# Kernel tuning notes

Hardware: AMD Instinct MI355X
Metric: run time of the kernel (lower is better)

## Reference

```python
import jax, jax.numpy as jnp
import numpy as np

B, E, R, A, NV, SEL = 512, 1024, 1024, 512, 196, 36

def _lstm_cell(x, h, c, Wih, bih, Whh, bhh):
    g = x @ Wih.T + bih + h @ Whh.T + bhh
    i, f, gg, o = jnp.split(g, 4, axis=1)  # torch gate order i,f,g,o
    c2 = jax.nn.sigmoid(f) * c + jax.nn.sigmoid(i) * jnp.tanh(gg)
    h2 = jax.nn.sigmoid(o) * jnp.tanh(c2)
    return h2, c2

def _attention(h, feats, p_feats, Wh, bh, Wa, ba):
    # feats: [B,S,R], p_feats: [B,S,A]
    att_h = h @ Wh.T + bh                       # [B,A]
    dot = jnp.tanh(p_feats + att_h[:, None, :])  # [B,S,A]
    scores = jnp.einsum('bsa,a->bs', dot, Wa[0]) + ba[0]
    w = jax.nn.softmax(scores, axis=1)
    return jnp.einsum('bs,bsd->bd', w, feats)

def setup_inputs() -> dict:
    key = jax.random.key(0)
    ks = jax.random.split(key, 32)
    s = 0.02
    inp = {
        'xt': jax.random.normal(ks[0], (B, E), jnp.float32),
        'fc_feats': jax.random.normal(ks[1], (B, R), jnp.float32),
        'att_feats': jax.random.normal(ks[2], (B, NV, R), jnp.float32),
        'p_att_feats': jax.random.normal(ks[3], (B, NV, A), jnp.float32),
        'state_h': jax.random.normal(ks[4], (2, B, R), jnp.float32),
        'state_c': jax.random.normal(ks[5], (2, B, R), jnp.float32),
        # att_lstm: input E + 2R
        'W_ih_att': jax.random.normal(ks[6], (4 * R, E + 2 * R), jnp.float32) * s,
        'b_ih_att': jnp.zeros((4 * R,), jnp.float32),
        'W_hh_att': jax.random.normal(ks[7], (4 * R, R), jnp.float32) * s,
        'b_hh_att': jnp.zeros((4 * R,), jnp.float32),
        # lang_lstm: input 3R
        'W_ih_lang': jax.random.normal(ks[8], (4 * R, 3 * R), jnp.float32) * s,
        'b_ih_lang': jnp.zeros((4 * R,), jnp.float32),
        'W_hh_lang': jax.random.normal(ks[9], (4 * R, R), jnp.float32) * s,
        'b_hh_lang': jnp.zeros((4 * R,), jnp.float32),
        # attention 1
        'Wh2att1': jax.random.normal(ks[10], (A, R), jnp.float32) * s,
        'bh2att1': jnp.zeros((A,), jnp.float32),
        'Walpha1': jax.random.normal(ks[11], (1, A), jnp.float32) * s,
        'balpha1': jnp.zeros((1,), jnp.float32),
        # vf attention
        'Wh2att2': jax.random.normal(ks[12], (A, R), jnp.float32) * s,
        'bh2att2': jnp.zeros((A,), jnp.float32),
        'Walpha2': jax.random.normal(ks[13], (1, A), jnp.float32) * s,
        'balpha2': jnp.zeros((1,), jnp.float32),
        # vf_layer and p_vf
        'W_vf': jax.random.normal(ks[14], (NV, 2 * R), jnp.float32) * s,
        'b_vf': jnp.zeros((NV,), jnp.float32),
        'W_pvf': jax.random.normal(ks[15], (A, R), jnp.float32) * s,
        'b_pvf': jnp.zeros((A,), jnp.float32),
    }
    return inp

def reference(xt, fc_feats, att_feats, p_att_feats, state_h, state_c,
              W_ih_att, b_ih_att, W_hh_att, b_hh_att,
              W_ih_lang, b_ih_lang, W_hh_lang, b_hh_lang,
              Wh2att1, bh2att1, Walpha1, balpha1,
              Wh2att2, bh2att2, Walpha2, balpha2,
              W_vf, b_vf, W_pvf, b_pvf):
    # dropout in eval mode -> identity
    prev_h = state_h[-1]
    att_lstm_input = jnp.concatenate([prev_h, fc_feats, xt], axis=1)
    h_att, c_att = _lstm_cell(att_lstm_input, state_h[0], state_c[0],
                              W_ih_att, b_ih_att, W_hh_att, b_hh_att)
    att = _attention(h_att, att_feats, p_att_feats, Wh2att1, bh2att1, Walpha1, balpha1)
    conc = jnp.concatenate([att, h_att], axis=1)          # [B,2R]
    vf_ha = conc @ W_vf.T + b_vf                          # [B,NV]
    vf_soft = jax.nn.softmax(vf_ha, axis=1)
    _, vf_ix = jax.lax.top_k(vf_soft, SEL)                # [B,SEL] (descending)
    arr1 = jnp.take_along_axis(att_feats, vf_ix[:, :, None], axis=1)  # [B,SEL,R]
    p_vf_feats = arr1 @ W_pvf.T + b_pvf                   # [B,SEL,A]
    vf_att = _attention(h_att, arr1, p_vf_feats, Wh2att2, bh2att2, Walpha2, balpha2)
    lang_lstm_input = jnp.concatenate([vf_att, h_att, att], axis=1)
    h_lang, c_lang = _lstm_cell(lang_lstm_input, state_h[1], state_c[1],
                                W_ih_lang, b_ih_lang, W_hh_lang, b_hh_lang)
    output = h_lang
    new_h = jnp.stack([h_att, h_lang])
    new_c = jnp.stack([c_att, c_lang])
    return output, new_h, new_c
```

## Files before the change

### kernel.cpp

```cpp
#include <hip/hip_runtime.h>

typedef __attribute__((ext_vector_type(4))) float f32x4;
typedef __attribute__((ext_vector_type(8))) _Float16 half8;
typedef __attribute__((ext_vector_type(4))) _Float16 half4;

__device__ __forceinline__ float fast_tanh(float x) {
  float e = __expf(2.f * x);
  return 1.f - 2.f / (e + 1.f);
}
__device__ __forceinline__ float fast_sigmoid(float x) {
  return 1.f / (1.f + __expf(-x));
}

__device__ __forceinline__ void gl_lds16(const _Float16* g, _Float16* l) {
  __builtin_amdgcn_global_load_lds(
      (const __attribute__((address_space(1))) void*)g,
      (__attribute__((address_space(3))) void*)l, 16, 0, 0);
}

template<int SPLIT, int OUT16, int NGUARD>
__global__ __launch_bounds__(256) void gemm16(
    const _Float16* __restrict__ Ahp, const _Float16* __restrict__ Alp, int lda,
    const _Float16* __restrict__ Bhp, const _Float16* __restrict__ Blp, int ldb,
    void* __restrict__ Cp, int ldc, long czstride,
    int N, int Kc)
{
  __shared__ _Float16 sAh[128 * 32];
  __shared__ _Float16 sBh[128 * 32];
  __shared__ _Float16 sAl[SPLIT == 3 ? 128 * 32 : 8];
  __shared__ _Float16 sBl[SPLIT == 3 ? 128 * 32 : 8];

  const int tid = threadIdx.x, lane = tid & 63, wid = tid >> 6;
  const int wm = wid >> 1, wn = wid & 1;
  const int l16 = lane & 15, k8 = lane >> 4;
  const int srow = lane >> 2;
  const int scol = (lane & 3) * 8;

  const int  kt0   = blockIdx.z * Kc;
  const long abase = (long)blockIdx.y * 128;
  const long bbase = (long)blockIdx.x * 128;

  const int r0 = wid * 32 + srow;
  const int r1 = wid * 32 + 16 + srow;
  long br0 = bbase + r0, br1 = bbase + r1;
  if (NGUARD) {
    if (br0 > N - 1) br0 = N - 1;
    if (br1 > N - 1) br1 = N - 1;
  }

  const _Float16* ga0 = Ahp + (abase + r0) * (long)lda + kt0 + scol;
  const _Float16* ga1 = Ahp + (abase + r1) * (long)lda + kt0 + scol;
  const _Float16* gb0 = Bhp + br0 * (long)ldb + kt0 + scol;
  const _Float16* gb1 = Bhp + br1 * (long)ldb + kt0 + scol;
  const _Float16* la0 = SPLIT == 3 ? Alp + (abase + r0) * (long)lda + kt0 + scol : nullptr;
  const _Float16* la1 = SPLIT == 3 ? Alp + (abase + r1) * (long)lda + kt0 + scol : nullptr;
  const _Float16* lb0 = SPLIT == 3 ? Blp + br0 * (long)ldb + kt0 + scol : nullptr;
  const _Float16* lb1 = SPLIT == 3 ? Blp + br1 * (long)ldb + kt0 + scol : nullptr;

  const int e0 = (wid * 32) * 32;
  const int e1 = (wid * 32 + 16) * 32;

  f32x4 acc[4][4];
#pragma unroll
  for (int i = 0; i < 4; i++)
#pragma unroll
    for (int j = 0; j < 4; j++) acc[i][j] = (f32x4){0.f, 0.f, 0.f, 0.f};

  for (int kk = 0; kk < Kc; kk += 32) {
    gl_lds16(ga0 + kk, sAh + e0);
    gl_lds16(ga1 + kk, sAh + e1);
    gl_lds16(gb0 + kk, sBh + e0);
    gl_lds16(gb1 + kk, sBh + e1);
    if (SPLIT == 3) {
      gl_lds16(la0 + kk, sAl + e0);
      gl_lds16(la1 + kk, sAl + e1);
      gl_lds16(lb0 + kk, sBl + e0);
      gl_lds16(lb1 + kk, sBl + e1);
    }
    __syncthreads();

    half8 ah[4], bh[4];
#pragma unroll
    for (int m = 0; m < 4; m++)
      ah[m] = *(const half8*)&sAh[(wm * 64 + m * 16 + l16) * 32 + k8 * 8];
#pragma unroll
    for (int n = 0; n < 4; n++)
      bh[n] = *(const half8*)&sBh[(wn * 64 + n * 16 + l16) * 32 + k8 * 8];
#pragma unroll
    for (int m = 0; m < 4; m++)
#pragma unroll
      for (int n = 0; n < 4; n++)
        acc[m][n] = __builtin_amdgcn_mfma_f32_16x16x32_f16(ah[m], bh[n], acc[m][n], 0, 0, 0);
    if (SPLIT == 3) {
      half8 al[4], bl[4];
#pragma unroll
      for (int m = 0; m < 4; m++)
        al[m] = *(const half8*)&sAl[(wm * 64 + m * 16 + l16) * 32 + k8 * 8];
#pragma unroll
      for (int n = 0; n < 4; n++)
        bl[n] = *(const half8*)&sBl[(wn * 64 + n * 16 + l16) * 32 + k8 * 8];
#pragma unroll
      for (int m = 0; m < 4; m++)
#pragma unroll
        for (int n = 0; n < 4; n++) {
          acc[m][n] = __builtin_amdgcn_mfma_f32_16x16x32_f16(al[m], bh[n], acc[m][n], 0, 0, 0);
          acc[m][n] = __builtin_amdgcn_mfma_f32_16x16x32_f16(ah[m], bl[n], acc[m][n], 0, 0, 0);
        }
    }
    __syncthreads();
  }

  const long czoff = (long)blockIdx.z * czstride;
#pragma unroll
  for (int m = 0; m < 4; m++)
#pragma unroll
    for (int n = 0; n < 4; n++) {
      const long row0 = abase + wm * 64 + m * 16 + (lane >> 4) * 4;
      const long col  = bbase + wn * 64 + n * 16 + l16;
      if (!NGUARD || col < N) {
#pragma unroll
        for (int j = 0; j < 4; j++) {
          if (OUT16) ((_Float16*)Cp)[(row0 + j) * (long)ldc + col + czoff] = (_Float16)acc[m][n][j];
          else       ((float*)Cp)[(row0 + j) * (long)ldc + col + czoff] = acc[m][n][j];
        }
      }
    }
}

__global__ __launch_bounds__(256) void pack_kernel(
    const float* __restrict__ xt, const float* __restrict__ fc,
    const float* __restrict__ sh,
    _Float16* __restrict__ X1h, _Float16* __restrict__ X1l)
{
  int i = blockIdx.x * 256 + threadIdx.x;
  int b = i >> 10, rr = i & 1023;
  long base = (long)b * 4096;
  float v[4];
  v[0] = sh[524288 + i];
  v[1] = fc[i];
  v[2] = xt[i];
  v[3] = sh[i];
#pragma unroll
  for (int j = 0; j < 4; j++) {
    _Float16 h = (_Float16)v[j];
    X1h[base + j * 1024 + rr] = h;
    X1l[base + j * 1024 + rr] = (_Float16)(v[j] - (float)h);
  }
}

__global__ __launch_bounds__(256) void convertA_kernel(
    const float* __restrict__ WihA, const float* __restrict__ WhhA,
    const float* __restrict__ Wh1, const float* __restrict__ Wh2,
    const float* __restrict__ Wvf, const float* __restrict__ Wpvf,
    _Float16* __restrict__ WcAh, _Float16* __restrict__ WcAl,
    _Float16* __restrict__ W12h, _Float16* __restrict__ Wvfh,
    _Float16* __restrict__ Wvfl, _Float16* __restrict__ Wpvfh)
{
  int bi = blockIdx.x, t = threadIdx.x;
  if (bi < 16384) {
    long e = ((long)bi * 256 + t) * 4;
    int row = (int)(e >> 12), col = (int)(e & 4095);
    const float* src = (col < 3072) ? WihA + (long)row * 3072 + col
                                    : WhhA + (long)row * 1024 + (col - 3072);
    f32x4 v = *(const f32x4*)src;
    half4 h, l;
#pragma unroll
    for (int j = 0; j < 4; j++) { h[j] = (_Float16)v[j]; l[j] = (_Float16)(v[j] - (float)h[j]); }
    *(half4*)&WcAh[e] = h;
    *(half4*)&WcAl[e] = l;
  } else if (bi < 17408) {
    long e = ((long)(bi - 16384) * 256 + t) * 4;
    int row = (int)(e >> 10), col = (int)(e & 1023);
    const float* src = (row < 512) ? Wh1 + (long)row * 1024 + col
                                   : Wh2 + (long)(row - 512) * 1024 + col;
    f32x4 v = *(const f32x4*)src;
    half4 h;
#pragma unroll
    for (int j = 0; j < 4; j++) h[j] = (_Float16)v[j];
    *(half4*)&W12h[e] = h;
  } else if (bi < 17800) {
    long e = ((long)(bi - 17408) * 256 + t) * 4;
    f32x4 v = *(const f32x4*)(Wvf + e);
    half4 h, l;
#pragma unroll
    for (int j = 0; j < 4; j++) { h[j] = (_Float16)v[j]; l[j] = (_Float16)(v[j] - (float)h[j]); }
    *(half4*)&Wvfh[e] = h;
    *(half4*)&Wvfl[e] = l;
  } else {
    long e = ((long)(bi - 17800) * 256 + t) * 4;
    f32x4 v = *(const f32x4*)(Wpvf + e);
    half4 h;
#pragma unroll
    for (int j = 0; j < 4; j++) h[j] = (_Float16)v[j];
    *(half4*)&Wpvfh[e] = h;
  }
}

__global__ __launch_bounds__(256) void convertL_kernel(
    const float* __restrict__ WihL, const float* __restrict__ WhhL,
    _Float16* __restrict__ WcLh)
{
  long e = ((long)blockIdx.x * 256 + threadIdx.x) * 4;
  int row = (int)(e >> 12), col = (int)(e & 4095);
  const float* src = (col < 3072) ? WihL + (long)row * 3072 + col
                                  : WhhL + (long)row * 1024 + (col - 3072);
  f32x4 v = *(const f32x4*)src;
  half4 h;
#pragma unroll
  for (int j = 0; j < 4; j++) h[j] = (_Float16)v[j];
  *(half4*)&WcLh[e] = h;
}

template<int NP, bool H16, bool ATT>
__global__ __launch_bounds__(256) void lstm_act_kernel(
    const void* __restrict__ gp, const float* __restrict__ bih,
    const float* __restrict__ bhh, const float* __restrict__ cin,
    float* __restrict__ hOut, float* __restrict__ cOut,
    _Float16* __restrict__ hatt_h, _Float16* __restrict__ conch,
    _Float16* __restrict__ concl, float* __restrict__ hOut2)
{
  const long S = 2097152;
  int i = blockIdx.x * 256 + threadIdx.x;
  int b = i >> 10, rr = i & 1023;
  long gb = (long)b * 4096;
  float g4[4];
#pragma unroll
  for (int q = 0; q < 4; q++) {
    float s = 0.f;
#pragma unroll
    for (int z = 0; z < NP; z++) {
      long off = (long)z * S + gb + q * 1024 + rr;
      s += H16 ? (float)((const _Float16*)gp)[off] : ((const float*)gp)[off];
    }
    g4[q] = s + bih[q * 1024 + rr] + bhh[q * 1024 + rr];
  }
  float c  = cin[i];
  float c2 = fast_sigmoid(g4[1]) * c + fast_sigmoid(g4[0]) * fast_tanh(g4[2]);
  float h2 = fast_sigmoid(g4[3]) * fast_tanh(c2);
  hOut[i] = h2;
  cOut[i] = c2;
  if (hOut2) hOut2[i] = h2;
  if (ATT) {
    _Float16 hh = (_Float16)h2;
    hatt_h[i] = hh;
    conch[(long)b * 2048 + 1024 + rr] = hh;
    concl[(long)b * 2048 + 1024 + rr] = (_Float16)(h2 - (float)hh);
  }
}

__global__ __launch_bounds__(256) void x2fill_kernel(
    const float* __restrict__ hatt, const float* __restrict__ sh,
    _Float16* __restrict__ x2h)
{
  int i = blockIdx.x * 256 + threadIdx.x;
  int b = i >> 10, rr = i & 1023;
  x2h[(long)b * 4096 + 1024 + rr] = (_Float16)hatt[i];
  x2h[(long)b * 4096 + 3072 + rr] = (_Float16)sh[524288 + i];
}

__global__ __launch_bounds__(256) void reduce_atth_kernel(
    const float* __restrict__ p, float* __restrict__ o)
{
  int i = (blockIdx.x * 256 + threadIdx.x) * 4;
  f32x4 a = *(const f32x4*)(p + i);
  f32x4 b = *(const f32x4*)(p + 524288 + i);
  f32x4 c = *(const f32x4*)(p + 1048576 + i);
  f32x4 d = *(const f32x4*)(p + 1572864 + i);
  *(f32x4*)(o + i) = a + b + c + d;
}

template<bool EXTRA, bool PF16>
__global__ __launch_bounds__(256) void score_kernel(
    const void* __restrict__ pf, const float* __restrict__ atth,
    const float* __restrict__ bh, const float* __restrict__ extra,
    const float* __restrict__ walpha, const float* __restrict__ balpha,
    float* __restrict__ out, int S, int nrows)
{
  int gw = blockIdx.x * 4 + (threadIdx.x >> 6);
  int lane = threadIdx.x & 63;
  if (gw >= nrows) return;
  int b = gw / S;
  const float* ah = atth + (long)b * 1024 + lane * 8;
  const float* bp = bh + lane * 8;
  const float* wp = walpha + lane * 8;
  const float* ep = EXTRA ? extra + lane * 8 : nullptr;
  float pv[8];
  if (PF16) {
    half8 hv = *(const half8*)((const _Float16*)pf + (long)gw * 512 + lane * 8);
#pragma unroll
    for (int j = 0; j < 8; j++) pv[j] = (float)hv[j];
  } else {
    const float* p = (const float*)pf + (long)gw * 512 + lane * 8;
#pragma unroll
    for (int u = 0; u < 2; u++) { f32x4 t = *(const f32x4*)(p + u * 4);
#pragma unroll
      for (int j = 0; j < 4; j++) pv[u * 4 + j] = t[j]; }
  }
  float acc = 0.f;
#pragma unroll
  for (int u = 0; u < 2; u++) {
    f32x4 av = *(const f32x4*)(ah + u * 4);
    f32x4 bv = *(const f32x4*)(bp + u * 4);
    f32x4 wv = *(const f32x4*)(wp + u * 4);
    f32x4 ev = EXTRA ? *(const f32x4*)(ep + u * 4) : (f32x4){0.f, 0.f, 0.f, 0.f};
#pragma unroll
    for (int j = 0; j < 4; j++) {
      float x = pv[u * 4 + j] + av[j] + bv[j] + ev[j];
      acc += fast_tanh(x) * wv[j];
    }
  }
#pragma unroll
  for (int off = 32; off; off >>= 1) acc += __shfl_xor(acc, off);
  if (lane == 0) out[gw] = acc + balpha[0];
}

__global__ __launch_bounds__(256) void attsum1_kernel(
    const float* __restrict__ scores, const float* __restrict__ feats,
    _Float16* __restrict__ conch, _Float16* __restrict__ concl, _Float16* __restrict__ x2h)
{
  __shared__ float w[256];
  int b = blockIdx.x, t = threadIdx.x;
  float s0 = (t < 196) ? scores[b * 196 + t] : -3.0e38f;
  w[t] = s0;
  __syncthreads();
  float mx = -3.0e38f;
  for (int i = 0; i < 196; i++) mx = fmaxf(mx, w[i]);
  float sum = 0.f;
  for (int i = 0; i < 196; i++) sum += __expf(w[i] - mx);
  float inv = 1.f / sum;
  __syncthreads();
  if (t < 196) w[t] = __expf(s0 - mx) * inv;
  __syncthreads();
  f32x4 acc = (f32x4){0.f, 0.f, 0.f, 0.f};
  const float* fb = feats + (long)b * 200704 + t * 4;
  for (int s0i = 0; s0i < 192; s0i += 8) {
    f32x4 v[8];
#pragma unroll
    for (int u = 0; u < 8; u++) v[u] = *(const f32x4*)(fb + (long)(s0i + u) * 1024);
#pragma unroll
    for (int u = 0; u < 8; u++) {
      float ws = w[s0i + u];
#pragma unroll
      for (int j = 0; j < 4; j++) acc[j] += ws * v[u][j];
    }
  }
#pragma unroll
  for (int u = 192; u < 196; u++) {
    float ws = w[u];
    f32x4 v = *(const f32x4*)(fb + (long)u * 1024);
#pragma unroll
    for (int j = 0; j < 4; j++) acc[j] += ws * v[j];
  }
  half4 h, l;
#pragma unroll
  for (int j = 0; j < 4; j++) { h[j] = (_Float16)acc[j]; l[j] = (_Float16)(acc[j] - (float)h[j]); }
  *(half4*)&conch[(long)b * 2048 + t * 4] = h;
  *(half4*)&concl[(long)b * 2048 + t * 4] = l;
  *(half4*)&x2h[(long)b * 4096 + 2048 + t * 4] = h;
}

__global__ __launch_bounds__(256) void attsum2_kernel(
    const float* __restrict__ scores, const _Float16* __restrict__ arr1h,
    _Float16* __restrict__ x2h)
{
  __shared__ float w[64];
  int b = blockIdx.x, t = threadIdx.x;
  if (t < 64) w[t] = (t < 36) ? scores[b * 36 + t] : -3.0e38f;
  __syncthreads();
  float mx = -3.0e38f;
  for (int i = 0; i < 36; i++) mx = fmaxf(mx, w[i]);
  float sum = 0.f;
  for (int i = 0; i < 36; i++) sum += __expf(w[i] - mx);
  float inv = 1.f / sum;
  __syncthreads();
  if (t < 36) w[t] = __expf(w[t] - mx) * inv;
  __syncthreads();
  f32x4 acc = (f32x4){0.f, 0.f, 0.f, 0.f};
  const _Float16* fb = arr1h + (long)b * 36 * 1024 + t * 4;
#pragma unroll 4
  for (int s = 0; s < 36; s++) {
    float ws = w[s];
    half4 v = *(const half4*)(fb + (long)s * 1024);
#pragma unroll
    for (int j = 0; j < 4; j++) acc[j] += ws * (float)v[j];
  }
  half4 h;
#pragma unroll
  for (int j = 0; j < 4; j++) h[j] = (_Float16)acc[j];
  *(half4*)&x2h[(long)b * 4096 + t * 4] = h;
}

__global__ __launch_bounds__(64) void topk_kernel(
    const float* __restrict__ vfp, const float* __restrict__ b_vf, int* __restrict__ ix)
{
  int b = blockIdx.x;
  int lane = threadIdx.x;
  float v[4];
#pragma unroll
  for (int j = 0; j < 4; j++) {
    int s = lane + 64 * j;
    float sum = -3.0e38f;
    if (s < 196) {
      sum = b_vf[s];
#pragma unroll
      for (int z = 0; z < 8; z++) sum += vfp[(long)z * 100352 + b * 196 + s];
    }
    v[j] = sum;
  }
  for (int it = 0; it < 36; it++) {
    float bv = -3.0e38f; int bs = 1 << 20;
#pragma unroll
    for (int j = 0; j < 4; j++) {
      int s = lane + 64 * j;
      if (v[j] > bv) { bv = v[j]; bs = s; }
    }
#pragma unroll
    for (int off = 32; off; off >>= 1) {
      float ov = __shfl_xor(bv, off);
      int   os = __shfl_xor(bs, off);
      if (ov > bv || (ov == bv && os < bs)) { bv = ov; bs = os; }
    }
    if ((bs & 63) == lane) v[bs >> 6] = -3.0e38f;
    if (lane == 0) ix[b * 36 + it] = bs;
  }
}

__global__ __launch_bounds__(256) void gather_conv_kernel(
    const float* __restrict__ feats, const int* __restrict__ ix, _Float16* __restrict__ dst)
{
  int bj = blockIdx.x;
  int b = bj / 36;
  int s = ix[bj];
  int t = threadIdx.x;
  f32x4 v = *(const f32x4*)(feats + ((long)b * 196 + s) * 1024 + t * 4);
  half4 h;
#pragma unroll
  for (int j = 0; j < 4; j++) h[j] = (_Float16)v[j];
  *(half4*)&dst[(long)bj * 1024 + t * 4] = h;
}

extern "C" void kernel_launch(void* const* d_in, const int* in_sizes, int n_in,
                              void* d_out, int out_size, void* d_ws, size_t ws_size,
                              hipStream_t stream) {
  const float* xt        = (const float*)d_in[0];
  const float* fc_feats  = (const float*)d_in[1];
  const float* att_feats = (const float*)d_in[2];
  const float* p_att     = (const float*)d_in[3];
  const float* state_h   = (const float*)d_in[4];
  const float* state_c   = (const float*)d_in[5];
  const float* b_ih_att  = (const float*)d_in[7];
  const float* b_hh_att  = (const float*)d_in[9];
  const float* b_ih_lang = (const float*)d_in[11];
  const float* b_hh_lang = (const float*)d_in[13];
  const float* bh2att1   = (const float*)d_in[15];
  const float* Walpha1   = (const float*)d_in[16];
  const float* balpha1   = (const float*)d_in[17];
  const float* bh2att2   = (const float*)d_in[19];
  const float* Walpha2   = (const float*)d_in[20];
  const float* balpha2   = (const float*)d_in[21];
  const float* b_vf      = (const float*)d_in[23];
  const float* b_pvf     = (const float*)d_in[25];

  float* out = (float*)d_out;
  float* W = (float*)d_ws;

  _Float16* WcAh   = (_Float16*)(W + 0);
  _Float16* WcAl   = (_Float16*)(W + 8388608);
  _Float16* X1h    = (_Float16*)(W + 16777216);
  _Float16* X1l    = (_Float16*)(W + 17825792);
  float*    g1p    = W + 18874368;
  _Float16* hatt_h = (_Float16*)(W + 27262976);
  _Float16* W12h   = (_Float16*)(W + 27525120);
  _Float16* Wvfh   = (_Float16*)(W + 28049408);
  _Float16* Wvfl   = (_Float16*)(W + 28250112);
  _Float16* Wpvfh  = (_Float16*)(W + 28450816);
  _Float16* WcLh   = WcAh;
  float*    vfhap  = W + 8388608;
  _Float16* arr1h  = (_Float16*)(W + 8388608);
  _Float16* g2ph   = (_Float16*)(W + 8388608);
  _Float16* conch  = (_Float16*)(W + 17825792);
  _Float16* concl  = (_Float16*)(W + 18350080);
  int*      vfix   = (int*)(W + 17825792);
  float*    scores2= W + 17844224;
  float*    atthp  = W + 18874368;
  float*    atth   = W + 20971520;
  _Float16* X2h    = (_Float16*)(W + 21495808);
  float*    scores1= W + 22544384;
  _Float16* pvf16  = (_Float16*)(W + 22544384);

  float* out_h0 = out + 524288;
  float* out_h1 = out + 2 * 524288;
  float* out_c0 = out + 3 * 524288;
  float* out_c1 = out + 4 * 524288;

  pack_kernel<<<2048, 256, 0, stream>>>(xt, fc_feats, state_h, X1h, X1l);

  convertA_kernel<<<18312, 256, 0, stream>>>(
      (const float*)d_in[6], (const float*)d_in[8],
      (const float*)d_in[14], (const float*)d_in[18],
      (const float*)d_in[22], (const float*)d_in[24],
      WcAh, WcAl, W12h, Wvfh, Wvfl, Wpvfh);

  gemm16<3, 0, 0><<<dim3(32, 4, 4), 256, 0, stream>>>(
      X1h, X1l, 4096, WcAh, WcAl, 4096, g1p, 4096, 2097152, 4096, 1024);

  lstm_act_kernel<4, false, true><<<2048, 256, 0, stream>>>(
      g1p, b_ih_att, b_hh_att, state_c, out_h0, out_c0,
      hatt_h, conch, concl, nullptr);

  x2fill_kernel<<<2048, 256, 0, stream>>>(out_h0, state_h, X2h);

  convertL_kernel<<<16384, 256, 0, stream>>>(
      (const float*)d_in[10], (const float*)d_in[12], WcLh);

  gemm16<1, 0, 0><<<dim3(8, 4, 4), 256, 0, stream>>>(
      hatt_h, nullptr, 1024, W12h, nullptr, 1024, atthp, 1024, 524288, 1024, 256);
  reduce_atth_kernel<<<512, 256, 0, stream>>>(atthp, atth);

  score_kernel<false, false><<<25088, 256, 0, stream>>>(
      p_att, atth, bh2att1, nullptr, Walpha1, balpha1, scores1, 196, 100352);

  attsum1_kernel<<<512, 256, 0, stream>>>(scores1, att_feats, conch, concl, X2h);

  gemm16<3, 0, 1><<<dim3(2, 4, 8), 256, 0, stream>>>(
      conch, concl, 2048, Wvfh, Wvfl, 2048, vfhap, 196, 100352, 196, 256);

  topk_kernel<<<512, 64, 0, stream>>>(vfhap, b_vf, vfix);

  gather_conv_kernel<<<18432, 256, 0, stream>>>(att_feats, vfix, arr1h);

  gemm16<1, 1, 0><<<dim3(4, 144, 1), 256, 0, stream>>>(
      arr1h, nullptr, 1024, Wpvfh, nullptr, 1024, pvf16, 512, 0, 512, 1024);

  score_kernel<true, true><<<4608, 256, 0, stream>>>(
      pvf16, atth + 512, bh2att2, b_pvf, Walpha2, balpha2, scores2, 36, 18432);

  attsum2_kernel<<<512, 256, 0, stream>>>(scores2, arr1h, X2h);

  gemm16<1, 1, 0><<<dim3(32, 4, 8), 256, 0, stream>>>(
      X2h, nullptr, 4096, WcLh, nullptr, 4096, g2ph, 4096, 2097152, 4096, 512);

  lstm_act_kernel<8, true, false><<<2048, 256, 0, stream>>>(
      g2ph, b_ih_lang, b_hh_lang, state_c + 524288, out, out_c1,
      nullptr, nullptr, nullptr, out_h1);
}
```

Before: 443.8 us.

## Add double-buffered full-M GEMM for LSTM gates, swizzle LDS, fuse vf attention

Adds a gemm_big kernel for the two big LSTM gate GEMMs. It uses 512 threads, a tile covering all 512 rows by 64 columns, double-buffered LDS staging and a 4-way K split, so each weight tile is read once and loads overlap the MFMA work. LDS column addressing is XOR-swizzled in both GEMMs to cut bank conflicts. The vf score and softmax-sum kernels are fused into one, and the vf GEMM split-K is raised from 8 to 16 with topk summing more partials. Other changes are a swapped grid order for the pvf GEMM and moving convertL earlier. Risks are lower occupancy from the large LDS footprint and more partial-sum traffic.

```diff
diff --git a/kernel.cpp b/kernel.cpp
--- a/kernel.cpp
+++ b/kernel.cpp
@@ -18,7 +18,107 @@
       (__attribute__((address_space(3))) void*)l, 16, 0, 0);
 }
 
-template<int SPLIT, int OUT16, int NGUARD>
+template<int SPLIT, int OUT16>
+__global__ __launch_bounds__(512, 2) void gemm_big(
+    const _Float16* __restrict__ Ahp, const _Float16* __restrict__ Alp,
+    const _Float16* __restrict__ Bhp, const _Float16* __restrict__ Blp,
+    int K, int Kc, void* __restrict__ Cp, long czstride)
+{
+  __shared__ _Float16 sAh[2][512 * 32];
+  __shared__ _Float16 sBh[2][64 * 32];
+  __shared__ _Float16 sAl[SPLIT == 3 ? 2 : 1][SPLIT == 3 ? 512 * 32 : 8];
+  __shared__ _Float16 sBl[SPLIT == 3 ? 2 : 1][SPLIT == 3 ? 64 * 32 : 8];
+
+  const int lane = threadIdx.x & 63, wid = threadIdx.x >> 6;
+  const int sr = lane >> 2;
+  const int sgr = (lane & 3) ^ ((lane >> 3) & 3);
+  const int l16 = lane & 15, k8 = lane >> 4;
+  const int koff = ((k8 ^ ((lane >> 1) & 3))) * 8;
+
+  const int  z     = blockIdx.x;
+  const long nbase = (long)blockIdx.y * 64;
+  const int  kt0   = z * Kc;
+
+  f32x4 acc[4][4];
+#pragma unroll
+  for (int i = 0; i < 4; i++)
+#pragma unroll
+    for (int j = 0; j < 4; j++) acc[i][j] = (f32x4){0.f, 0.f, 0.f, 0.f};
+
+  auto STAGE = [&](int buf, int kt) {
+#pragma unroll
+    for (int g = 0; g < 4; g++) {
+      const int rloc = wid * 64 + g * 16 + sr;
+      gl_lds16(Ahp + (long)rloc * K + kt + sgr * 8, &sAh[buf][(wid * 64 + g * 16) * 32]);
+      if (SPLIT == 3)
+        gl_lds16(Alp + (long)rloc * K + kt + sgr * 8, &sAl[buf][(wid * 64 + g * 16) * 32]);
+    }
+    if (wid < 4) {
+      const int rloc = wid * 16 + sr;
+      gl_lds16(Bhp + (nbase + rloc) * K + kt + sgr * 8, &sBh[buf][(wid * 16) * 32]);
+    } else if (SPLIT == 3) {
+      const int rloc = (wid - 4) * 16 + sr;
+      gl_lds16(Blp + (nbase + rloc) * K + kt + sgr * 8, &sBl[buf][((wid - 4) * 16) * 32]);
+    }
+  };
+
+  STAGE(0, kt0);
+  __syncthreads();
+
+  int buf = 0;
+  const int nst = Kc >> 5;
+  for (int t = 0; t < nst; t++) {
+    if (t + 1 < nst) STAGE(buf ^ 1, kt0 + (t + 1) * 32);
+
+    half8 ah[4], bh[4];
+#pragma unroll
+    for (int m = 0; m < 4; m++)
+      ah[m] = *(const half8*)&sAh[buf][(wid * 64 + m * 16 + l16) * 32 + koff];
+#pragma unroll
+    for (int n = 0; n < 4; n++)
+      bh[n] = *(const half8*)&sBh[buf][(n * 16 + l16) * 32 + koff];
+#pragma unroll
+    for (int m = 0; m < 4; m++)
+#pragma unroll
+      for (int n = 0; n < 4; n++)
+        acc[m][n] = __builtin_amdgcn_mfma_f32_16x16x32_f16(ah[m], bh[n], acc[m][n], 0, 0, 0);
+    if (SPLIT == 3) {
+      half8 al[4], bl[4];
+#pragma unroll
+      for (int m = 0; m < 4; m++)
+        al[m] = *(const half8*)&sAl[buf][(wid * 64 + m * 16 + l16) * 32 + koff];
+#pragma unroll
+      for (int n = 0; n < 4; n++)
+        bl[n] = *(const half8*)&sBl[buf][(n * 16 + l16) * 32 + koff];
+#pragma unroll
+      for (int m = 0; m < 4; m++)
+#pragma unroll
+        for (int n = 0; n < 4; n++) {
+          acc[m][n] = __builtin_amdgcn_mfma_f32_16x16x32_f16(al[m], bh[n], acc[m][n], 0, 0, 0);
+          acc[m][n] = __builtin_amdgcn_mfma_f32_16x16x32_f16(ah[m], bl[n], acc[m][n], 0, 0, 0);
+        }
+    }
+    __syncthreads();
+    buf ^= 1;
+  }
+
+  const long czoff = (long)z * czstride;
+#pragma unroll
+  for (int m = 0; m < 4; m++)
+#pragma unroll
+    for (int n = 0; n < 4; n++) {
+      const long row0 = wid * 64 + m * 16 + (lane >> 4) * 4;
+      const long col  = nbase + n * 16 + l16;
+#pragma unroll
+      for (int j = 0; j < 4; j++) {
+        const long idx = czoff + (row0 + j) * 4096 + col;
+        if (OUT16) ((_Float16*)Cp)[idx] = (_Float16)acc[m][n][j];
+        else       ((float*)Cp)[idx] = acc[m][n][j];
+      }
+    }
+}
+
+template<int SPLIT, int OUT16, int NGUARD, int SWAPXY>
 __global__ __launch_bounds__(256) void gemm16(
     const _Float16* __restrict__ Ahp, const _Float16* __restrict__ Alp, int lda,
     const _Float16* __restrict__ Bhp, const _Float16* __restrict__ Blp, int ldb,
@@ -33,15 +133,16 @@
   const int tid = threadIdx.x, lane = tid & 63, wid = tid >> 6;
   const int wm = wid >> 1, wn = wid & 1;
   const int l16 = lane & 15, k8 = lane >> 4;
-  const int srow = lane >> 2;
-  const int scol = (lane & 3) * 8;
+  const int sr = lane >> 2;
+  const int scol = ((lane & 3) ^ ((lane >> 3) & 3)) * 8;
+  const int koff = ((k8 ^ ((lane >> 1) & 3))) * 8;
 
   const int  kt0   = blockIdx.z * Kc;
-  const long abase = (long)blockIdx.y * 128;
-  const long bbase = (long)blockIdx.x * 128;
-
-  const int r0 = wid * 32 + srow;
-  const int r1 = wid * 32 + 16 + srow;
+  const long abase = (long)(SWAPXY ? blockIdx.x : blockIdx.y) * 128;
+  const long bbase = (long)(SWAPXY ? blockIdx.y : blockIdx.x) * 128;
+
+  const int r0 = wid * 32 + sr;
+  const int r1 = wid * 32 + 16 + sr;
   long br0 = bbase + r0, br1 = bbase + r1;
   if (NGUARD) {
     if (br0 > N - 1) br0 = N - 1;
@@ -82,10 +183,10 @@
     half8 ah[4], bh[4];
 #pragma unroll
     for (int m = 0; m < 4; m++)
-      ah[m] = *(const half8*)&sAh[(wm * 64 + m * 16 + l16) * 32 + k8 * 8];
+      ah[m] = *(const half8*)&sAh[(wm * 64 + m * 16 + l16) * 32 + koff];
 #pragma unroll
     for (int n = 0; n < 4; n++)
-      bh[n] = *(const half8*)&sBh[(wn * 64 + n * 16 + l16) * 32 + k8 * 8];
+      bh[n] = *(const half8*)&sBh[(wn * 64 + n * 16 + l16) * 32 + koff];
 #pragma unroll
     for (int m = 0; m < 4; m++)
 #pragma unroll
@@ -95,10 +196,10 @@
       half8 al[4], bl[4];
 #pragma unroll
       for (int m = 0; m < 4; m++)
-        al[m] = *(const half8*)&sAl[(wm * 64 + m * 16 + l16) * 32 + k8 * 8];
+        al[m] = *(const half8*)&sAl[(wm * 64 + m * 16 + l16) * 32 + koff];
 #pragma unroll
       for (int n = 0; n < 4; n++)
-        bl[n] = *(const half8*)&sBl[(wn * 64 + n * 16 + l16) * 32 + k8 * 8];
+        bl[n] = *(const half8*)&sBl[(wn * 64 + n * 16 + l16) * 32 + koff];
 #pragma unroll
       for (int m = 0; m < 4; m++)
 #pragma unroll
@@ -120,8 +221,9 @@
       if (!NGUARD || col < N) {
 #pragma unroll
         for (int j = 0; j < 4; j++) {
-          if (OUT16) ((_Float16*)Cp)[(row0 + j) * (long)ldc + col + czoff] = (_Float16)acc[m][n][j];
-          else       ((float*)Cp)[(row0 + j) * (long)ldc + col + czoff] = acc[m][n][j];
+          const long idx = (row0 + j) * (long)ldc + col + czoff;
+          if (OUT16) ((_Float16*)Cp)[idx] = (_Float16)acc[m][n][j];
+          else       ((float*)Cp)[idx] = acc[m][n][j];
         }
       }
     }
@@ -269,45 +371,30 @@
   *(f32x4*)(o + i) = a + b + c + d;
 }
 
-template<bool EXTRA, bool PF16>
-__global__ __launch_bounds__(256) void score_kernel(
-    const void* __restrict__ pf, const float* __restrict__ atth,
-    const float* __restrict__ bh, const float* __restrict__ extra,
+__global__ __launch_bounds__(256) void score1_kernel(
+    const float* __restrict__ pf, const float* __restrict__ atth,
+    const float* __restrict__ bh,
     const float* __restrict__ walpha, const float* __restrict__ balpha,
-    float* __restrict__ out, int S, int nrows)
+    float* __restrict__ out, int nrows)
 {
   int gw = blockIdx.x * 4 + (threadIdx.x >> 6);
   int lane = threadIdx.x & 63;
   if (gw >= nrows) return;
-  int b = gw / S;
+  int b = gw / 196;
+  const float* p  = pf + (long)gw * 512 + lane * 8;
   const float* ah = atth + (long)b * 1024 + lane * 8;
   const float* bp = bh + lane * 8;
   const float* wp = walpha + lane * 8;
-  const float* ep = EXTRA ? extra + lane * 8 : nullptr;
-  float pv[8];
-  if (PF16) {
-    half8 hv = *(const half8*)((const _Float16*)pf + (long)gw * 512 + lane * 8);
-#pragma unroll
-    for (int j = 0; j < 8; j++) pv[j] = (float)hv[j];
-  } else {
-    const float* p = (const float*)pf + (long)gw * 512 + lane * 8;
-#pragma unroll
-    for (int u = 0; u < 2; u++) { f32x4 t = *(const f32x4*)(p + u * 4);
-#pragma unroll
-      for (int j = 0; j < 4; j++) pv[u * 4 + j] = t[j]; }
-  }
   float acc = 0.f;
 #pragma unroll
   for (int u = 0; u < 2; u++) {
+    f32x4 pv = *(const f32x4*)(p + u * 4);
     f32x4 av = *(const f32x4*)(ah + u * 4);
     f32x4 bv = *(const f32x4*)(bp + u * 4);
     f32x4 wv = *(const f32x4*)(wp + u * 4);
-    f32x4 ev = EXTRA ? *(const f32x4*)(ep + u * 4) : (f32x4){0.f, 0.f, 0.f, 0.f};
-#pragma unroll
-    for (int j = 0; j < 4; j++) {
-      float x = pv[u * 4 + j] + av[j] + bv[j] + ev[j];
-      acc += fast_tanh(x) * wv[j];
-    }
+#pragma unroll
+    for (int j = 0; j < 4; j++)
+      acc += fast_tanh(pv[j] + av[j] + bv[j]) * wv[j];
   }
 #pragma unroll
   for (int off = 32; off; off >>= 1) acc += __shfl_xor(acc, off);
@@ -359,13 +446,33 @@
   *(half4*)&x2h[(long)b * 4096 + 2048 + t * 4] = h;
 }
 
-__global__ __launch_bounds__(256) void attsum2_kernel(
-    const float* __restrict__ scores, const _Float16* __restrict__ arr1h,
-    _Float16* __restrict__ x2h)
-{
-  __shared__ float w[64];
-  int b = blockIdx.x, t = threadIdx.x;
-  if (t < 64) w[t] = (t < 36) ? scores[b * 36 + t] : -3.0e38f;
+__global__ __launch_bounds__(256) void vfatt_kernel(
+    const _Float16* __restrict__ pvf16, const float* __restrict__ atth2,
+    const float* __restrict__ bh2att2, const float* __restrict__ b_pvf,
+    const float* __restrict__ walpha2, const float* __restrict__ balpha2,
+    const _Float16* __restrict__ arr1h, _Float16* __restrict__ x2h)
+{
+  __shared__ float w[40];
+  int b = blockIdx.x, tid = threadIdx.x;
+  int lane = tid & 63, wv = tid >> 6;
+
+  float add[8], wal[8];
+#pragma unroll
+  for (int u = 0; u < 8; u++) {
+    int a = lane * 8 + u;
+    add[u] = atth2[(long)b * 1024 + a] + bh2att2[a] + b_pvf[a];
+    wal[u] = walpha2[a];
+  }
+  for (int j = wv; j < 36; j += 4) {
+    half8 hv = *(const half8*)&pvf16[((long)b * 36 + j) * 512 + lane * 8];
+    float acc = 0.f;
+#pragma unroll
+    for (int u = 0; u < 8; u++)
+      acc += fast_tanh((float)hv[u] + add[u]) * wal[u];
+#pragma unroll
+    for (int off = 32; off; off >>= 1) acc += __shfl_xor(acc, off);
+    if (lane == 0) w[j] = acc + balpha2[0];
+  }
   __syncthreads();
   float mx = -3.0e38f;
   for (int i = 0; i < 36; i++) mx = fmaxf(mx, w[i]);
@@ -373,10 +480,10 @@
   for (int i = 0; i < 36; i++) sum += __expf(w[i] - mx);
   float inv = 1.f / sum;
   __syncthreads();
-  if (t < 36) w[t] = __expf(w[t] - mx) * inv;
+  if (tid < 36) w[tid] = __expf(w[tid] - mx) * inv;
   __syncthreads();
   f32x4 acc = (f32x4){0.f, 0.f, 0.f, 0.f};
-  const _Float16* fb = arr1h + (long)b * 36 * 1024 + t * 4;
+  const _Float16* fb = arr1h + (long)b * 36 * 1024 + tid * 4;
 #pragma unroll 4
   for (int s = 0; s < 36; s++) {
     float ws = w[s];
@@ -387,9 +494,10 @@
   half4 h;
 #pragma unroll
   for (int j = 0; j < 4; j++) h[j] = (_Float16)acc[j];
-  *(half4*)&x2h[(long)b * 4096 + t * 4] = h;
-}
-
+  *(half4*)&x2h[(long)b * 4096 + tid * 4] = h;
+}
+
+template<int NP>
 __global__ __launch_bounds__(64) void topk_kernel(
     const float* __restrict__ vfp, const float* __restrict__ b_vf, int* __restrict__ ix)
 {
@@ -403,7 +511,7 @@
     if (s < 196) {
       sum = b_vf[s];
 #pragma unroll
-      for (int z = 0; z < 8; z++) sum += vfp[(long)z * 100352 + b * 196 + s];
+      for (int z = 0; z < NP; z++) sum += vfp[(long)z * 100352 + b * 196 + s];
     }
     v[j] = sum;
   }
@@ -481,7 +589,6 @@
   _Float16* conch  = (_Float16*)(W + 17825792);
   _Float16* concl  = (_Float16*)(W + 18350080);
   int*      vfix   = (int*)(W + 17825792);
-  float*    scores2= W + 17844224;
   float*    atthp  = W + 18874368;
   float*    atth   = W + 20971520;
   _Float16* X2h    = (_Float16*)(W + 21495808);
@@ -501,8 +608,11 @@
       (const float*)d_in[22], (const float*)d_in[24],
       WcAh, WcAl, W12h, Wvfh, Wvfl, Wpvfh);
 
-  gemm16<3, 0, 0><<<dim3(32, 4, 4), 256, 0, stream>>>(
-      X1h, X1l, 4096, WcAh, WcAl, 4096, g1p, 4096, 2097152, 4096, 1024);
+  gemm_big<3, 0><<<dim3(4, 64), 512, 0, stream>>>(
+      X1h, X1l, WcAh, WcAl, 4096, 1024, g1p, 2097152);
+
+  convertL_kernel<<<16384, 256, 0, stream>>>(
+      (const float*)d_in[10], (const float*)d_in[12], WcLh);
 
   lstm_act_kernel<4, false, true><<<2048, 256, 0, stream>>>(
       g1p, b_ih_att, b_hh_att, state_c, out_h0, out_c0,
@@ -510,37 +620,32 @@
 
   x2fill_kernel<<<2048, 256, 0, stream>>>(out_h0, state_h, X2h);
 
-  convertL_kernel<<<16384, 256, 0, stream>>>(
-      (const float*)d_in[10], (const float*)d_in[12], WcLh);
-
-  gemm16<1, 0, 0><<<dim3(8, 4, 4), 256, 0, stream>>>(
+  gemm16<1, 0, 0, 0><<<dim3(8, 4, 4), 256, 0, stream>>>(
       hatt_h, nullptr, 1024, W12h, nullptr, 1024, atthp, 1024, 524288, 1024, 256);
   reduce_atth_kernel<<<512, 256, 0, stream>>>(atthp, atth);
 
-  score_kernel<false, false><<<25088, 256, 0, stream>>>(
-      p_att, atth, bh2att1, nullptr, Walpha1, balpha1, scores1, 196, 100352);
+  score1_kernel<<<25088, 256, 0, stream>>>(
+      p_att, atth, bh2att1, Walpha1, balpha1, scores1, 100352);
 
   attsum1_kernel<<<512, 256, 0, stream>>>(scores1, att_feats, conch, concl, X2h);
 
-  gemm16<3, 0, 1><<<dim3(2, 4, 8), 256, 0, stream>>>(
-      conch, concl, 2048, Wvfh, Wvfl, 2048, vfhap, 196, 100352, 196, 256);
-
-  topk_kernel<<<512, 64, 0, stream>>>(vfhap, b_vf, vfix);
+  gemm16<3, 0, 1, 0><<<dim3(2, 4, 16), 256, 0, stream>>>(
+      conch, concl, 2048, Wvfh, Wvfl, 2048, vfhap, 196, 100352, 196, 128);
+
+  topk_kernel<16><<<512, 64, 0, stream>>>(vfhap, b_vf, vfix);
 
   gather_conv_kernel<<<18432, 256, 0, stream>>>(att_feats, vfix, arr1h);
 
-  gemm16<1, 1, 0><<<dim3(4, 144, 1), 256, 0, stream>>>(
+  gemm16<1, 1, 0, 1><<<dim3(144, 4, 1), 256, 0, stream>>>(
       arr1h, nullptr, 1024, Wpvfh, nullptr, 1024, pvf16, 512, 0, 512, 1024);
 
-  score_kernel<true, true><<<4608, 256, 0, stream>>>(
-      pvf16, atth + 512, bh2att2, b_pvf, Walpha2, balpha2, scores2, 36, 18432);
-
-  attsum2_kernel<<<512, 256, 0, stream>>>(scores2, arr1h, X2h);
-
-  gemm16<1, 1, 0><<<dim3(32, 4, 8), 256, 0, stream>>>(
-      X2h, nullptr, 4096, WcLh, nullptr, 4096, g2ph, 4096, 2097152, 4096, 512);
-
-  lstm_act_kernel<8, true, false><<<2048, 256, 0, stream>>>(
+  vfatt_kernel<<<512, 256, 0, stream>>>(
+      pvf16, atth + 512, bh2att2, b_pvf, Walpha2, balpha2, arr1h, X2h);
+
+  gemm_big<1, 1><<<dim3(4, 64), 512, 0, stream>>>(
+      X2h, nullptr, WcLh, nullptr, 4096, 1024, g2ph, 2097152);
+
+  lstm_act_kernel<4, true, false><<<2048, 256, 0, stream>>>(
       g2ph, b_ih_lang, b_hh_lang, state_c + 524288, out, out_c1,
       nullptr, nullptr, nullptr, out_h1);
 }
```

Measured after the change: 466.4 us. 5.1% more time.
